# Kernel optimization log

Hardware: AMD Instinct MI355X
Metric: run time of the kernel (lower is better)

## Reference

```python
import jax, jax.numpy as jnp
import numpy as np

DIM = 1024
DFF = 4096
B, L = 4, 4096


def _lin_init(key, din, dout):
    k1, k2 = jax.random.split(key)
    bound = 1.0 / np.sqrt(din)
    w = jax.random.uniform(k1, (din, dout), jnp.float32, -bound, bound)
    b = jax.random.uniform(k2, (dout,), jnp.float32, -bound, bound)
    return w, b


def setup_inputs() -> dict:
    key = jax.random.key(0)
    ks = jax.random.split(key, 12)
    x = jax.random.normal(ks[0], (B, L, DIM), jnp.float32)
    hidden = jax.random.normal(ks[1], (B, DIM), jnp.float32)
    w_ln_z, b_ln_z = _lin_init(ks[2], DIM, DIM)
    w_dt, b_dt = _lin_init(ks[3], DIM, DIM)
    w_y, b_y = _lin_init(ks[4], DIM, DIM)
    w_yg, b_yg = _lin_init(ks[5], DIM, DIM)
    w_ff, b_ff = _lin_init(ks[6], DIM, DFF)
    w_ffg, b_ffg = _lin_init(ks[7], DIM, DFF)
    w_ffo, b_ffo = _lin_init(ks[8], DFF, DIM)
    g_sio = jnp.ones((DIM,), jnp.float32)
    g_ffn = jnp.ones((DIM,), jnp.float32)
    return dict(x=x, hidden=hidden, w_ln_z=w_ln_z, b_ln_z=b_ln_z, w_dt=w_dt,
                b_dt=b_dt, w_y=w_y, b_y=b_y, w_yg=w_yg, b_yg=b_yg,
                w_ff=w_ff, b_ff=b_ff, w_ffg=w_ffg, b_ffg=b_ffg,
                w_ffo=w_ffo, b_ffo=b_ffo, g_sio=g_sio, g_ffn=g_ffn)


def _rmsnorm(x, g, eps=1e-6):
    return x * jax.lax.rsqrt(jnp.mean(x * x, axis=-1, keepdims=True) + eps) * g


def reference(x, hidden, w_ln_z, b_ln_z, w_dt, b_dt, w_y, b_y, w_yg, b_yg,
              w_ff, b_ff, w_ffg, b_ffg, w_ffo, b_ffo, g_sio, g_ffn):
    silu = jax.nn.silu
    sp = jax.nn.softplus
    # --- SioConv branch ---
    residual = x
    xn = _rmsnorm(x, g_sio)
    dt = xn @ w_dt + b_dt
    ln_z = -sp(-(xn @ w_ln_z + b_ln_z))
    ln_da = -sp(-dt)           # log sigmoid(dt)
    ln_o_da = -sp(dt)          # log sigmoid(-dt)
    ln_o_da_cumsum = jnp.cumsum(ln_o_da, axis=1)
    lcse = jax.lax.cumlogsumexp(ln_z + ln_da - ln_o_da_cumsum, axis=1)
    h_inner = jnp.exp(lcse + ln_o_da_cumsum)                 # [B,L,D]
    h_cross = jnp.exp(ln_o_da_cumsum) * hidden[:, None, :]   # [B,L,D]
    h = h_inner + h_cross
    y = (h @ w_y + b_y) * silu(xn @ w_yg + b_yg)
    x = y + residual
    # --- FFN branch ---
    residual = x
    xn = _rmsnorm(x, g_ffn)
    ff = ((xn @ w_ff + b_ff) * silu(xn @ w_ffg + b_ffg)) @ w_ffo + b_ffo
    x = ff + residual
    return (x, h)
```

## Files before the change

### kernel.cpp

```cpp
#include <hip/hip_runtime.h>
#include <cstdint>
#include <cstddef>

using u16 = unsigned short;
using bf16x8 = __attribute__((ext_vector_type(8))) short;
using f32x4  = __attribute__((ext_vector_type(4))) float;

__device__ __forceinline__ u16 f2bf(float f) {
  unsigned u = __float_as_uint(f);
  u += 0x7fffu + ((u >> 16) & 1u);
  return (u16)(u >> 16);
}
__device__ __forceinline__ float bf2f(u16 h) {
  return __uint_as_float(((unsigned)h) << 16);
}

__device__ __forceinline__ void gload_lds16(const void* g, void* l) {
  auto gp = reinterpret_cast<const __attribute__((address_space(1))) char*>(
      reinterpret_cast<uintptr_t>(g));
  auto lp = reinterpret_cast<__attribute__((address_space(3))) char*>(
      reinterpret_cast<uintptr_t>(l));
  __builtin_amdgcn_global_load_lds(gp, lp, 16, 0, 0);
}

__global__ __launch_bounds__(256) void transpose_to_bf16(
    const float* __restrict__ W, u16* __restrict__ WT, int din, int dout) {
  __shared__ float tile[32][33];
  const int j0 = blockIdx.x * 32;
  const int i0 = blockIdx.y * 32;
  const int tx = threadIdx.x & 31;
  const int ty = threadIdx.x >> 5;
#pragma unroll
  for (int k = 0; k < 32; k += 8)
    tile[ty + k][tx] = W[(size_t)(i0 + ty + k) * dout + (j0 + tx)];
  __syncthreads();
#pragma unroll
  for (int k = 0; k < 32; k += 8)
    WT[(size_t)(j0 + ty + k) * din + (i0 + tx)] = f2bf(tile[tx][ty + k]);
}

__global__ __launch_bounds__(256) void rmsnorm_kernel(
    const float* __restrict__ x, const float* __restrict__ g, u16* __restrict__ xn) {
  const int row = blockIdx.x;
  const float4 v = ((const float4*)(x + (size_t)row * 1024))[threadIdx.x];
  float ss = v.x * v.x + v.y * v.y + v.z * v.z + v.w * v.w;
#pragma unroll
  for (int off = 32; off > 0; off >>= 1) ss += __shfl_down(ss, off, 64);
  __shared__ float red[4];
  if ((threadIdx.x & 63) == 0) red[threadIdx.x >> 6] = ss;
  __syncthreads();
  const float rs = rsqrtf((red[0] + red[1] + red[2] + red[3]) * (1.f / 1024.f) + 1e-6f);
  const float4 gv = ((const float4*)g)[threadIdx.x];
  ushort4 o;
  o.x = f2bf(v.x * rs * gv.x);
  o.y = f2bf(v.y * rs * gv.y);
  o.z = f2bf(v.z * rs * gv.z);
  o.w = f2bf(v.w * rs * gv.w);
  ((ushort4*)(xn + (size_t)row * 1024))[threadIdx.x] = o;
}

__global__ __launch_bounds__(256) void scan_pass1(
    const u16* __restrict__ dt, const u16* __restrict__ lnz,
    float* __restrict__ P, float* __restrict__ S) {
  const int blk = blockIdx.x;
  const int dblk = blk & 3;
  const int chunk = (blk >> 2) & 63;
  const int b = blk >> 8;
  const int d = dblk * 256 + threadIdx.x;
  const size_t base = ((size_t)b * 4096 + (size_t)chunk * 64) * 1024 + d;
  float p = 1.f, s = 0.f;
#pragma unroll 8
  for (int l = 0; l < 64; ++l) {
    const float dtv = bf2f(dt[base + (size_t)l * 1024]);
    const float zv = bf2f(lnz[base + (size_t)l * 1024]);
    const float a = 1.f / (1.f + __expf(dtv));
    const float zs = 1.f / (1.f + __expf(-zv));
    const float in = (1.f - a) * zs;
    p *= a;
    s = a * s + in;
  }
  const size_t o = ((size_t)b * 64 + chunk) * 1024 + d;
  P[o] = p;
  S[o] = s;
}

__global__ __launch_bounds__(256) void scan_pass2(
    const float* __restrict__ P, const float* __restrict__ S,
    const float* __restrict__ hidden, float* __restrict__ hin) {
  const int idx = blockIdx.x * 256 + threadIdx.x;
  const int b = idx >> 10, d = idx & 1023;
  float h = hidden[idx];
#pragma unroll 8
  for (int c = 0; c < 64; ++c) {
    const size_t o = ((size_t)b * 64 + c) * 1024 + d;
    hin[o] = h;
    h = P[o] * h + S[o];
  }
}

__global__ __launch_bounds__(256) void scan_pass3(
    const u16* __restrict__ dt, const u16* __restrict__ lnz,
    const float* __restrict__ hin, float* __restrict__ h_out, u16* __restrict__ hbf) {
  const int blk = blockIdx.x;
  const int dblk = blk & 3;
  const int chunk = (blk >> 2) & 63;
  const int b = blk >> 8;
  const int d = dblk * 256 + threadIdx.x;
  const size_t base = ((size_t)b * 4096 + (size_t)chunk * 64) * 1024 + d;
  float h = hin[((size_t)b * 64 + chunk) * 1024 + d];
#pragma unroll 4
  for (int l = 0; l < 64; ++l) {
    const float dtv = bf2f(dt[base + (size_t)l * 1024]);
    const float zv = bf2f(lnz[base + (size_t)l * 1024]);
    const float a = 1.f / (1.f + __expf(dtv));
    const float zs = 1.f / (1.f + __expf(-zv));
    h = a * h + (1.f - a) * zs;
    h_out[base + (size_t)l * 1024] = h;
    hbf[base + (size_t)l * 1024] = f2bf(h);
  }
}

template <int EPI>
__global__ __launch_bounds__(512) void gemm256(
    const u16* __restrict__ A, const u16* __restrict__ B,
    const float* __restrict__ bias, const u16* __restrict__ gate,
    const float* __restrict__ resid, float* __restrict__ outF,
    u16* __restrict__ outH, u16* __restrict__ outH2, u16* __restrict__ outH3,
    int ntx, int N, int K) {
  constexpr int SLOT = 16384;
  constexpr int LDSZ = 10 * SLOT;
  const int tid = threadIdx.x;
  const int lane = tid & 63;
  const int wid = tid >> 6;
  const int wr = wid >> 2;
  const int wc = wid & 3;

  const int nwg = gridDim.x;
  int id = blockIdx.x;
  id = (id & 7) * (nwg >> 3) + (id >> 3);
  const int m0 = (id / ntx) * 256;
  const int n0 = (id % ntx) * 256;

  __shared__ __align__(16) char lds[LDSZ];

  f32x4 acc[8][4];
#pragma unroll
  for (int m = 0; m < 8; ++m)
#pragma unroll
    for (int n = 0; n < 4; ++n) acc[m][n] = (f32x4){0.f, 0.f, 0.f, 0.f};

  bf16x8 aR[4][2], bR[4][2];

  int aOff[4][2], bOff[2][2];
  {
    const int lq = (lane >> 4) << 4;
#pragma unroll
    for (int m = 0; m < 4; ++m) {
      const int hr = m * 16 + (lane & 15);
#pragma unroll
      for (int k = 0; k < 2; ++k)
        aOff[m][k] = hr * 128 + ((k * 64 + lq) ^ ((hr & 7) << 4));
    }
#pragma unroll
    for (int n = 0; n < 2; ++n) {
      const int hr = (wc & 1) * 64 + n * 16 + (lane & 15);
#pragma unroll
      for (int k = 0; k < 2; ++k)
        bOff[n][k] = hr * 128 + ((k * 64 + lq) ^ ((hr & 7) << 4));
    }
  }

  const int row0 = tid >> 3;
  const int kb0  = ((tid & 7) * 16) ^ ((row0 & 7) << 4);
  const size_t dRow = (size_t)128 * K;
  const char* pA0 = (const char*)A + (size_t)(m0 + row0) * K * 2 + kb0;
  const char* pA1 = pA0 + (size_t)256 * K;
  const char* pB0 = (const char*)B + (size_t)(n0 + row0) * K * 2 + kb0;
  const char* pB1 = pB0 + (size_t)256 * K;
  const int ldst = tid * 16;

#define STAGE(PTR, SB)                                                        \
  {                                                                           \
    gload_lds16(PTR, lds + (SB) + ldst);                                      \
    gload_lds16(PTR + dRow, lds + (SB) + ldst + 8192);                        \
    PTR += 128;                                                               \
  }

#define READA(SAB, QM)                                                        \
  _Pragma("unroll") for (int m = 0; m < 4; ++m)                               \
  _Pragma("unroll") for (int k = 0; k < 2; ++k)                               \
    aR[m][k] = *(const bf16x8*)(lds + (SAB) + aOff[m][k] + (QM) * 8192);

#define READB(SBB, NP)                                                        \
  _Pragma("unroll") for (int n = 0; n < 2; ++n)                               \
  _Pragma("unroll") for (int k = 0; k < 2; ++k)                               \
    bR[(NP) + n][k] = *(const bf16x8*)(lds + (SBB) + bOff[n][k] + (NP) * 2048);

#define MMAQ(QM, QN)                                                          \
  __builtin_amdgcn_s_setprio(1);                                              \
  _Pragma("unroll") for (int m = 0; m < 4; ++m)                               \
  _Pragma("unroll") for (int n = 0; n < 2; ++n)                               \
  _Pragma("unroll") for (int k = 0; k < 2; ++k)                               \
      acc[(QM) * 4 + m][(QN) * 2 + n] = __builtin_amdgcn_mfma_f32_16x16x32_bf16( \
          aR[m][k], bR[(QN) * 2 + n][k], acc[(QM) * 4 + m][(QN) * 2 + n], 0, 0, 0); \
  __builtin_amdgcn_s_setprio(0);

  const int NT = K >> 6;

  STAGE(pA0, 0 * SLOT);
  STAGE(pA1, 1 * SLOT);
  STAGE(pB0, 2 * SLOT);
  STAGE(pB1, 3 * SLOT);
  STAGE(pA0, 4 * SLOT);
  STAGE(pA1, 5 * SLOT);
  STAGE(pB0, 6 * SLOT);
  asm volatile("s_waitcnt vmcnt(6)" ::: "memory");
  __builtin_amdgcn_s_barrier();

  int iA = wr;
  int iB = 2 + (wc >> 1);
  int iS = 7;

  for (int t = 0; t < NT; ++t) {
    const int sAb = __builtin_amdgcn_readfirstlane(iA * SLOT);
    const int sBb = __builtin_amdgcn_readfirstlane(iB * SLOT);
    int s0 = iS * SLOT;
    int s1 = s0 + SLOT; if (s1 >= LDSZ) s1 -= LDSZ;
    int s2 = s1 + SLOT; if (s2 >= LDSZ) s2 -= LDSZ;
    int s3 = s2 + SLOT; if (s3 >= LDSZ) s3 -= LDSZ;
    const bool st0 = (t <= NT - 2);
    const bool st123 = (t <= NT - 3);
    READA(sAb, 0);
    READB(sBb, 0);
    if (st0) STAGE(pB1, s0);
    MMAQ(0, 0);
    READB(sBb, 2);
    if (st123) STAGE(pA0, s1);
    MMAQ(0, 1);
    READA(sAb, 1);
    if (st123) STAGE(pA1, s2);
    MMAQ(1, 0);
    __builtin_amdgcn_s_barrier();
    if (st123) STAGE(pB0, s3);
    MMAQ(1, 1);
    if (t < NT - 2) asm volatile("s_waitcnt vmcnt(6)" ::: "memory");
    else            asm volatile("s_waitcnt vmcnt(0)" ::: "memory");
    __builtin_amdgcn_s_barrier();
    iA += 4; if (iA >= 10) iA -= 10;
    iB += 4; if (iB >= 10) iB -= 10;
    iS += 4; if (iS >= 10) iS -= 10;
  }

#pragma unroll
  for (int m = 0; m < 8; ++m) {
#pragma unroll
    for (int n = 0; n < 4; ++n) {
      const int col = n0 + wc * 64 + n * 16 + (lane & 15);
#pragma unroll
      for (int j = 0; j < 4; ++j) {
        const int row = m0 + wr * 128 + m * 16 + ((lane >> 4) << 2) + j;
        const float v = acc[m][n][j] + bias[col];
        if constexpr (EPI == 5) {
          const int rg = col >> 10;
          const size_t o = (size_t)row * 1024 + (col & 1023);
          if (rg == 0) outH[o] = f2bf(v);
          else if (rg == 1) outH2[o] = f2bf(v);
          else outH3[o] = f2bf(v);
        } else {
          const size_t o = (size_t)row * N + col;
          if constexpr (EPI == 2) {
            const float gt = bf2f(gate[o]);
            outF[o] = v * (gt / (1.f + __expf(-gt))) + resid[o];
          } else if constexpr (EPI == 6) {
            outH[o] = f2bf(v / (1.f + __expf(-v)));
          } else if constexpr (EPI == 7) {
            outH[o] = f2bf(v * bf2f(gate[o]));
          } else if constexpr (EPI == 4) {
            outF[o] = v + outF[o];
          }
        }
      }
    }
  }
#undef STAGE
#undef READA
#undef READB
#undef MMAQ
}

extern "C" void kernel_launch(void* const* d_in, const int* in_sizes, int n_in,
                              void* d_out, int out_size, void* d_ws, size_t ws_size,
                              hipStream_t stream) {
  const float* x      = (const float*)d_in[0];
  const float* hidden = (const float*)d_in[1];
  const float* w_ln_z = (const float*)d_in[2];
  const float* b_ln_z = (const float*)d_in[3];
  const float* w_dt   = (const float*)d_in[4];
  const float* b_dt   = (const float*)d_in[5];
  const float* w_y    = (const float*)d_in[6];
  const float* b_y    = (const float*)d_in[7];
  const float* w_yg   = (const float*)d_in[8];
  const float* b_yg   = (const float*)d_in[9];
  const float* w_ff   = (const float*)d_in[10];
  const float* b_ff   = (const float*)d_in[11];
  const float* w_ffg  = (const float*)d_in[12];
  const float* b_ffg  = (const float*)d_in[13];
  const float* w_ffo  = (const float*)d_in[14];
  const float* b_ffo  = (const float*)d_in[15];
  const float* g_sio  = (const float*)d_in[16];
  const float* g_ffn  = (const float*)d_in[17];

  char* ws = (char*)d_ws;
  const size_t MB = 1ull << 20;
  u16*   WT_cat = (u16*)(ws + 0 * MB);
  u16*   WT_y   = (u16*)(ws + 8 * MB);
  u16*   WT_ff  = (u16*)(ws + 10 * MB);
  u16*   WT_ffg = (u16*)(ws + 18 * MB);
  u16*   WT_ffo = (u16*)(ws + 26 * MB);
  float* b_cat  = (float*)(ws + 34 * MB);
  u16*   xn     = (u16*)(ws + 36 * MB);
  u16*   dt16   = (u16*)(ws + 68 * MB);
  u16*   lnzb   = (u16*)(ws + 100 * MB);
  u16*   ygb    = (u16*)(ws + 132 * MB);
  u16*   hbf    = (u16*)(ws + 164 * MB);
  float* Pc     = (float*)(ws + 196 * MB);
  float* Sc     = (float*)(ws + 197 * MB);
  float* hin    = (float*)(ws + 198 * MB);
  u16*   gs     = (u16*)(ws + 68 * MB);

  float* x_out = (float*)d_out;
  float* h_out = (float*)d_out + (size_t)4 * 4096 * 1024;

  const int M = 16384, D = 1024, F = 4096;
  const dim3 tb(256);

  transpose_to_bf16<<<dim3(32, 32), tb, 0, stream>>>(w_dt, WT_cat, D, D);
  transpose_to_bf16<<<dim3(32, 32), tb, 0, stream>>>(w_ln_z, WT_cat + 1024 * 1024, D, D);
  transpose_to_bf16<<<dim3(32, 32), tb, 0, stream>>>(w_yg, WT_cat + 2 * 1024 * 1024, D, D);
  transpose_to_bf16<<<dim3(32, 32), tb, 0, stream>>>(w_y, WT_y, D, D);
  transpose_to_bf16<<<dim3(128, 32), tb, 0, stream>>>(w_ff, WT_ff, D, F);
  transpose_to_bf16<<<dim3(128, 32), tb, 0, stream>>>(w_ffg, WT_ffg, D, F);
  transpose_to_bf16<<<dim3(32, 128), tb, 0, stream>>>(w_ffo, WT_ffo, F, D);
  (void)hipMemcpyAsync(b_cat, b_dt, D * 4, hipMemcpyDeviceToDevice, stream);
  (void)hipMemcpyAsync(b_cat + 1024, b_ln_z, D * 4, hipMemcpyDeviceToDevice, stream);
  (void)hipMemcpyAsync(b_cat + 2048, b_yg, D * 4, hipMemcpyDeviceToDevice, stream);

  rmsnorm_kernel<<<M, tb, 0, stream>>>(x, g_sio, xn);

  gemm256<5><<<dim3(12 * 64), 512, 0, stream>>>(xn, WT_cat, b_cat, nullptr, nullptr,
                                                nullptr, dt16, lnzb, ygb, 12, 3072, D);

  scan_pass1<<<1024, tb, 0, stream>>>(dt16, lnzb, Pc, Sc);
  scan_pass2<<<16, tb, 0, stream>>>(Pc, Sc, hidden, hin);
  scan_pass3<<<1024, tb, 0, stream>>>(dt16, lnzb, hin, h_out, hbf);

  gemm256<2><<<dim3(4 * 64), 512, 0, stream>>>(hbf, WT_y, b_y, ygb, x,
                                               x_out, nullptr, nullptr, nullptr, 4, D, D);

  rmsnorm_kernel<<<M, tb, 0, stream>>>(x_out, g_ffn, xn);

  gemm256<6><<<dim3(16 * 64), 512, 0, stream>>>(xn, WT_ffg, b_ffg, nullptr, nullptr,
                                                nullptr, gs, nullptr, nullptr, 16, F, D);
  gemm256<7><<<dim3(16 * 64), 512, 0, stream>>>(xn, WT_ff, b_ff, gs, nullptr,
                                                nullptr, gs, nullptr, nullptr, 16, F, D);
  gemm256<4><<<dim3(4 * 64), 512, 0, stream>>>(gs, WT_ffo, b_ffo, nullptr, nullptr,
                                               x_out, nullptr, nullptr, nullptr, 4, D, F);
}
```

Measured before the change: 759.6 us.

## Switch GEMM inner loop from 16x16x32 to 32x32x16 bf16 MFMA tiles

Rewrites the 256x256 GEMM's per-wave compute to use 32x32x16 MFMA instructions, with 32x32 accumulator tiles, re-derived LDS read offsets and a matching epilogue row/column mapping. Larger MFMA tiles need fewer LDS fragment reads per FLOP and fewer instructions per k-step. Both B fragments are now read up front, which raises register pressure. It also adds a launch_bounds min-blocks hint of 2 that may constrain register allocation and cause spills.

```diff
diff --git a/kernel.cpp b/kernel.cpp
--- a/kernel.cpp
+++ b/kernel.cpp
@@ -4,7 +4,7 @@
 
 using u16 = unsigned short;
 using bf16x8 = __attribute__((ext_vector_type(8))) short;
-using f32x4  = __attribute__((ext_vector_type(4))) float;
+using f32x16 = __attribute__((ext_vector_type(16))) float;
 
 __device__ __forceinline__ u16 f2bf(float f) {
   unsigned u = __float_as_uint(f);
@@ -121,7 +121,7 @@
 }
 
 template <int EPI>
-__global__ __launch_bounds__(512) void gemm256(
+__global__ __launch_bounds__(512, 2) void gemm256(
     const u16* __restrict__ A, const u16* __restrict__ B,
     const float* __restrict__ bias, const u16* __restrict__ gate,
     const float* __restrict__ resid, float* __restrict__ outF,
@@ -143,30 +143,33 @@
 
   __shared__ __align__(16) char lds[LDSZ];
 
-  f32x4 acc[8][4];
-#pragma unroll
-  for (int m = 0; m < 8; ++m)
-#pragma unroll
-    for (int n = 0; n < 4; ++n) acc[m][n] = (f32x4){0.f, 0.f, 0.f, 0.f};
-
-  bf16x8 aR[4][2], bR[4][2];
-
-  int aOff[4][2], bOff[2][2];
+  f32x16 acc[4][2];
+#pragma unroll
+  for (int m = 0; m < 4; ++m)
+#pragma unroll
+    for (int n = 0; n < 2; ++n)
+#pragma unroll
+      for (int j = 0; j < 16; ++j) acc[m][n][j] = 0.f;
+
+  bf16x8 aR[2][4];
+  bf16x8 bR[2][4];
+
+  int aOff[2][4], bOff[2][4];
   {
-    const int lq = (lane >> 4) << 4;
-#pragma unroll
-    for (int m = 0; m < 4; ++m) {
-      const int hr = m * 16 + (lane & 15);
-#pragma unroll
-      for (int k = 0; k < 2; ++k)
-        aOff[m][k] = hr * 128 + ((k * 64 + lq) ^ ((hr & 7) << 4));
+    const int lq = (lane >> 5) << 4;
+#pragma unroll
+    for (int mt = 0; mt < 2; ++mt) {
+      const int hr = mt * 32 + (lane & 31);
+#pragma unroll
+      for (int ks = 0; ks < 4; ++ks)
+        aOff[mt][ks] = hr * 128 + ((ks * 32 + lq) ^ ((hr & 7) << 4));
     }
 #pragma unroll
-    for (int n = 0; n < 2; ++n) {
-      const int hr = (wc & 1) * 64 + n * 16 + (lane & 15);
-#pragma unroll
-      for (int k = 0; k < 2; ++k)
-        bOff[n][k] = hr * 128 + ((k * 64 + lq) ^ ((hr & 7) << 4));
+    for (int nt = 0; nt < 2; ++nt) {
+      const int hr = (wc & 1) * 64 + nt * 32 + (lane & 31);
+#pragma unroll
+      for (int ks = 0; ks < 4; ++ks)
+        bOff[nt][ks] = hr * 128 + ((ks * 32 + lq) ^ ((hr & 7) << 4));
     }
   }
 
@@ -187,25 +190,23 @@
   }
 
 #define READA(SAB, QM)                                                        \
-  _Pragma("unroll") for (int m = 0; m < 4; ++m)                               \
-  _Pragma("unroll") for (int k = 0; k < 2; ++k)                               \
-    aR[m][k] = *(const bf16x8*)(lds + (SAB) + aOff[m][k] + (QM) * 8192);
-
-#define READB(SBB, NP)                                                        \
-  _Pragma("unroll") for (int n = 0; n < 2; ++n)                               \
-  _Pragma("unroll") for (int k = 0; k < 2; ++k)                               \
-    bR[(NP) + n][k] = *(const bf16x8*)(lds + (SBB) + bOff[n][k] + (NP) * 2048);
+  _Pragma("unroll") for (int mt = 0; mt < 2; ++mt)                            \
+  _Pragma("unroll") for (int ks = 0; ks < 4; ++ks)                            \
+    aR[mt][ks] = *(const bf16x8*)(lds + (SAB) + aOff[mt][ks] + (QM) * 8192);
+
+#define READB(SBB, NT)                                                        \
+  _Pragma("unroll") for (int ks = 0; ks < 4; ++ks)                            \
+    bR[NT][ks] = *(const bf16x8*)(lds + (SBB) + bOff[NT][ks]);
 
 #define MMAQ(QM, QN)                                                          \
   __builtin_amdgcn_s_setprio(1);                                              \
-  _Pragma("unroll") for (int m = 0; m < 4; ++m)                               \
-  _Pragma("unroll") for (int n = 0; n < 2; ++n)                               \
-  _Pragma("unroll") for (int k = 0; k < 2; ++k)                               \
-      acc[(QM) * 4 + m][(QN) * 2 + n] = __builtin_amdgcn_mfma_f32_16x16x32_bf16( \
-          aR[m][k], bR[(QN) * 2 + n][k], acc[(QM) * 4 + m][(QN) * 2 + n], 0, 0, 0); \
+  _Pragma("unroll") for (int mt = 0; mt < 2; ++mt)                            \
+  _Pragma("unroll") for (int ks = 0; ks < 4; ++ks)                            \
+      acc[(QM) * 2 + mt][QN] = __builtin_amdgcn_mfma_f32_32x32x16_bf16(       \
+          aR[mt][ks], bR[QN][ks], acc[(QM) * 2 + mt][QN], 0, 0, 0);           \
   __builtin_amdgcn_s_setprio(0);
 
-  const int NT = K >> 6;
+  const int NT2 = K >> 6;
 
   STAGE(pA0, 0 * SLOT);
   STAGE(pA1, 1 * SLOT);
@@ -221,20 +222,20 @@
   int iB = 2 + (wc >> 1);
   int iS = 7;
 
-  for (int t = 0; t < NT; ++t) {
+  for (int t = 0; t < NT2; ++t) {
     const int sAb = __builtin_amdgcn_readfirstlane(iA * SLOT);
     const int sBb = __builtin_amdgcn_readfirstlane(iB * SLOT);
     int s0 = iS * SLOT;
     int s1 = s0 + SLOT; if (s1 >= LDSZ) s1 -= LDSZ;
     int s2 = s1 + SLOT; if (s2 >= LDSZ) s2 -= LDSZ;
     int s3 = s2 + SLOT; if (s3 >= LDSZ) s3 -= LDSZ;
-    const bool st0 = (t <= NT - 2);
-    const bool st123 = (t <= NT - 3);
+    const bool st0 = (t <= NT2 - 2);
+    const bool st123 = (t <= NT2 - 3);
     READA(sAb, 0);
     READB(sBb, 0);
+    READB(sBb, 1);
     if (st0) STAGE(pB1, s0);
     MMAQ(0, 0);
-    READB(sBb, 2);
     if (st123) STAGE(pA0, s1);
     MMAQ(0, 1);
     READA(sAb, 1);
@@ -243,8 +244,8 @@
     __builtin_amdgcn_s_barrier();
     if (st123) STAGE(pB0, s3);
     MMAQ(1, 1);
-    if (t < NT - 2) asm volatile("s_waitcnt vmcnt(6)" ::: "memory");
-    else            asm volatile("s_waitcnt vmcnt(0)" ::: "memory");
+    if (t < NT2 - 2) asm volatile("s_waitcnt vmcnt(6)" ::: "memory");
+    else             asm volatile("s_waitcnt vmcnt(0)" ::: "memory");
     __builtin_amdgcn_s_barrier();
     iA += 4; if (iA >= 10) iA -= 10;
     iB += 4; if (iB >= 10) iB -= 10;
@@ -252,14 +253,14 @@
   }
 
 #pragma unroll
-  for (int m = 0; m < 8; ++m) {
-#pragma unroll
-    for (int n = 0; n < 4; ++n) {
-      const int col = n0 + wc * 64 + n * 16 + (lane & 15);
-#pragma unroll
-      for (int j = 0; j < 4; ++j) {
-        const int row = m0 + wr * 128 + m * 16 + ((lane >> 4) << 2) + j;
-        const float v = acc[m][n][j] + bias[col];
+  for (int mt = 0; mt < 4; ++mt) {
+#pragma unroll
+    for (int nt = 0; nt < 2; ++nt) {
+      const int col = n0 + wc * 64 + nt * 32 + (lane & 31);
+#pragma unroll
+      for (int reg = 0; reg < 16; ++reg) {
+        const int row = m0 + wr * 128 + mt * 32 + (reg & 3) + 8 * (reg >> 2) + 4 * (lane >> 5);
+        const float v = acc[mt][nt][reg] + bias[col];
         if constexpr (EPI == 5) {
           const int rg = col >> 10;
           const size_t o = (size_t)row * 1024 + (col & 1023);
```

Result: slower. 824.1 us (+8.5%).
